# Optimization experiments

Measured on AMD Instinct MI355X. Metric: run time of the kernel, lower is better.

The kernel has to match this reference:

```python
import jax, jax.numpy as jnp
import numpy as np


def _base_grid(B, H, W):
    xs = jnp.arange(W, dtype=jnp.float32)
    ys = jnp.arange(H, dtype=jnp.float32)
    gx, gy = jnp.meshgrid(xs, ys)  # [H,W] each, x varies along W
    return jnp.broadcast_to(jnp.stack([gx, gy], -1)[None], (B, H, W, 2))


def flow_to_grid(flow, accel=None):
    B, _, H, W = flow.shape
    v = 0.5 * flow
    if accel is not None:
        v = v + 0.25 * accel
    vgrid = _base_grid(B, H, W) + jnp.transpose(v, (0, 2, 3, 1))
    gx = 2.0 * vgrid[..., 0] / max(W - 1, 1) - 1.0
    gy = 2.0 * vgrid[..., 1] / max(H - 1, 1) - 1.0
    return jnp.stack([gx, gy], -1)  # [B,H,W,2]


def grid_sample_border(img, grid):
    # img [B,C,H,W], grid [B,Hg,Wg,2] normalized; bilinear, border pad, align_corners=True
    B, C, H, W = img.shape
    Hg, Wg = grid.shape[1], grid.shape[2]
    x = jnp.clip((grid[..., 0] + 1.0) * 0.5 * (W - 1), 0.0, W - 1)
    y = jnp.clip((grid[..., 1] + 1.0) * 0.5 * (H - 1), 0.0, H - 1)
    x0 = jnp.floor(x); y0 = jnp.floor(y)
    x1 = jnp.minimum(x0 + 1.0, W - 1); y1 = jnp.minimum(y0 + 1.0, H - 1)
    wx = (x - x0)[:, None]; wy = (y - y0)[:, None]  # [B,1,Hg,Wg]
    x0i, x1i, y0i, y1i = (a.astype(jnp.int32) for a in (x0, x1, y0, y1))
    flat = img.reshape(B, C, H * W)

    def gat(yi, xi):
        idx = jnp.broadcast_to((yi * W + xi).reshape(B, 1, Hg * Wg), (B, C, Hg * Wg))
        return jnp.take_along_axis(flat, idx, axis=2).reshape(B, C, Hg, Wg)

    v00, v01, v10, v11 = gat(y0i, x0i), gat(y0i, x1i), gat(y1i, x0i), gat(y1i, x1i)
    return v00 * (1 - wx) * (1 - wy) + v01 * wx * (1 - wy) + v10 * (1 - wx) * wy + v11 * wx * wy


def backward_warp(img, flow, accel=None):
    grid = flow_to_grid(flow, accel)
    warped = grid_sample_border(img, grid)
    valid = (jnp.abs(grid[..., 0]) <= 1.0) & (jnp.abs(grid[..., 1]) <= 1.0)
    return warped * valid[:, None].astype(img.dtype)


def local_kernel_warp(img, flow, kernel_params):
    B, C, H, W = img.shape
    k_row = jax.nn.softmax(kernel_params[:, :5], axis=1)   # [B,5,H,W]
    k_col = jax.nn.softmax(kernel_params[:, 5:10], axis=1)
    aniso = jax.nn.sigmoid(kernel_params[:, 10]) + 0.5     # [B,H,W]
    grid = flow_to_grid(flow)                               # [B,H,W,2]
    offsets = jnp.linspace(-2.0, 2.0, 5)
    a3 = aniso[..., None]                                   # [B,H,W,1]
    off_col = offsets.reshape(1, 1, 1, 5) * a3              # [B,H,W,5]
    off_row = offsets.reshape(1, 1, 1, 5) / a3
    zeros = jnp.zeros_like(off_row)
    grid_row = grid[:, :, :, None, :] + jnp.stack([off_row, zeros], -1) * (2.0 / W)
    samples_row = grid_sample_border(img, grid_row.reshape(B, H, W * 5, 2)).reshape(B, C, H, W, 5)
    img_row = jnp.einsum('bchwk,bkhw->bchw', samples_row, k_row)
    grid_base = flow_to_grid(jnp.zeros_like(flow))
    grid_col = grid_base[:, :, :, None, :] + jnp.stack([zeros, off_col], -1) * (2.0 / H)
    samples_col = grid_sample_border(img_row, grid_col.reshape(B, H, W * 5, 2)).reshape(B, C, H, W, 5)
    return jnp.einsum('bchwk,bkhw->bchw', samples_col, k_col)


def conv3x3(x, w, b):
    y = jax.lax.conv_general_dilated(x, w, (1, 1), 'SAME',
                                     dimension_numbers=('NCHW', 'OIHW', 'NCHW'))
    return y + b[None, :, None, None]


def reference(img, features, flow, kernel_params, w1, b1, w2, b2):
    B, _, H, W = img.shape
    Hf, Wf = features.shape[2], features.shape[3]
    warped_img = local_kernel_warp(img, flow, kernel_params)
    flow_scaled = jax.image.resize(flow, (B, 2, Hf, Wf), 'linear') * (Hf / H)
    warped_feat = backward_warp(features, flow_scaled)
    warped_img_down = jax.image.resize(warped_img, (B, 3, Hf, Wf), 'linear')
    x = jnp.concatenate([warped_feat, warped_img_down], axis=1)
    fused = conv3x3(jax.nn.relu(conv3x3(x, w1, b1)), w2, b2)
    return (warped_feat + fused, warped_img)


def setup_inputs() -> dict:
    key = jax.random.key(0)
    ks = jax.random.split(key, 6)
    B, H, W, Hf, Wf, Cf = 4, 512, 512, 256, 256, 96
    return {
        'img': jax.random.uniform(ks[0], (B, 3, H, W), jnp.float32),
        'features': jax.random.normal(ks[1], (B, Cf, Hf, Wf), jnp.float32),
        'flow': jax.random.normal(ks[2], (B, 2, H, W), jnp.float32) * 4.0,
        'kernel_params': jax.random.normal(ks[3], (B, 11, H, W), jnp.float32),
        'w1': jax.random.normal(ks[4], (Cf, Cf + 3, 3, 3), jnp.float32) * 0.02,
        'b1': jnp.zeros((Cf,), jnp.float32),
        'w2': jax.random.normal(ks[5], (Cf, Cf, 3, 3), jnp.float32) * 0.02,
        'b2': jnp.zeros((Cf,), jnp.float32),
    }
```

## Files before the change

### kernel.cpp

```cpp
#include <hip/hip_runtime.h>

#define NB 4
#define IH 512
#define IW 512
#define FH 256
#define FW 256
#define CF 96
#define C1 99
#define HWI (IH*IW)
#define HWF (FH*FW)

typedef short s8v __attribute__((ext_vector_type(8)));
typedef short s4v __attribute__((ext_vector_type(4)));
typedef float f4v __attribute__((ext_vector_type(4)));
typedef float f2v __attribute__((ext_vector_type(2), aligned(4)));

static __device__ __forceinline__ float sigmoidf_(float x) {
    return 1.0f / (1.0f + __expf(-x));
}
static __device__ __forceinline__ unsigned short f2bf(float f) {
    unsigned int u = __float_as_uint(f);
    unsigned int r = (u + 0x7fffu + ((u >> 16) & 1u)) >> 16;
    return (unsigned short)r;
}
static __device__ __forceinline__ float bf2f(short s) {
    unsigned int u = ((unsigned int)(unsigned short)s) << 16;
    return __uint_as_float(u);
}
static __device__ __forceinline__ void gl_lds16(const short* g, short* l) {
    __builtin_amdgcn_global_load_lds(
        (const __attribute__((address_space(1))) void*)g,
        (__attribute__((address_space(3))) void*)l, 16, 0, 0);
}

__global__ __launch_bounds__(256)
void lkw_row_kernel(const float* __restrict__ img,
                    const float* __restrict__ flow,
                    const float* __restrict__ kp,
                    float* __restrict__ img_row) {
    int idx = blockIdx.x * blockDim.x + threadIdx.x;
    if (idx >= NB * HWI) return;
    int w = idx & (IW - 1);
    int h = (idx >> 9) & (IH - 1);
    int b = idx >> 18;

    const float* kpb = kp + (size_t)b * 11 * HWI + h * IW + w;
    float p[5];
    float m = -1e30f;
    #pragma unroll
    for (int k = 0; k < 5; k++) { p[k] = kpb[k * HWI]; m = fmaxf(m, p[k]); }
    float s = 0.f;
    #pragma unroll
    for (int k = 0; k < 5; k++) { p[k] = __expf(p[k] - m); s += p[k]; }
    float invs = 1.f / s;
    float a = sigmoidf_(kpb[10 * HWI]) + 0.5f;
    float inva = 1.f / a;

    float fx = flow[((size_t)b * 2 + 0) * HWI + h * IW + w];
    float fy = flow[((size_t)b * 2 + 1) * HWI + h * IW + w];

    float y = (float)h + 0.5f * fy;
    y = fminf(fmaxf(y, 0.f), (float)(IH - 1));
    float y0f = floorf(y);
    int y0 = (int)y0f;
    int y1 = min(y0 + 1, IH - 1);
    float wy = y - y0f;

    float xbase = (float)w + 0.5f * fx;
    const float sc = (float)(IW - 1) / (float)IW;

    const float* imb = img + (size_t)b * 3 * HWI;
    float acc0 = 0.f, acc1 = 0.f, acc2 = 0.f;
    #pragma unroll
    for (int k = 0; k < 5; k++) {
        float x = xbase + (float)(k - 2) * inva * sc;
        x = fminf(fmaxf(x, 0.f), (float)(IW - 1));
        float x0f = floorf(x);
        int x0 = (int)x0f;
        int x1 = min(x0 + 1, IW - 1);
        float wx = x - x0f;
        float wk = p[k] * invs;
        float w00 = (1.f - wx) * (1.f - wy) * wk;
        float w01 = wx * (1.f - wy) * wk;
        float w10 = (1.f - wx) * wy * wk;
        float w11 = wx * wy * wk;
        int i00 = y0 * IW + x0, i01 = y0 * IW + x1;
        int i10 = y1 * IW + x0, i11 = y1 * IW + x1;
        acc0 += w00 * imb[i00] + w01 * imb[i01] + w10 * imb[i10] + w11 * imb[i11];
        acc1 += w00 * imb[HWI + i00] + w01 * imb[HWI + i01] + w10 * imb[HWI + i10] + w11 * imb[HWI + i11];
        acc2 += w00 * imb[2 * HWI + i00] + w01 * imb[2 * HWI + i01] + w10 * imb[2 * HWI + i10] + w11 * imb[2 * HWI + i11];
    }
    img_row[(size_t)b * 3 * HWI + h * IW + w] = acc0;
    img_row[(size_t)b * 3 * HWI + HWI + h * IW + w] = acc1;
    img_row[(size_t)b * 3 * HWI + 2 * HWI + h * IW + w] = acc2;
}

__global__ __launch_bounds__(256)
void lkw_col_kernel(const float* __restrict__ img_row,
                    const float* __restrict__ kp,
                    float* __restrict__ out1) {
    int idx = blockIdx.x * blockDim.x + threadIdx.x;
    if (idx >= NB * HWI) return;
    int w = idx & (IW - 1);
    int h = (idx >> 9) & (IH - 1);
    int b = idx >> 18;

    const float* kpb = kp + (size_t)b * 11 * HWI + h * IW + w;
    float p[5];
    float m = -1e30f;
    #pragma unroll
    for (int k = 0; k < 5; k++) { p[k] = kpb[(5 + k) * HWI]; m = fmaxf(m, p[k]); }
    float s = 0.f;
    #pragma unroll
    for (int k = 0; k < 5; k++) { p[k] = __expf(p[k] - m); s += p[k]; }
    float invs = 1.f / s;
    float a = sigmoidf_(kpb[10 * HWI]) + 0.5f;

    const float sc = (float)(IH - 1) / (float)IH;
    const float* irb = img_row + (size_t)b * 3 * HWI;
    float acc0 = 0.f, acc1 = 0.f, acc2 = 0.f;
    #pragma unroll
    for (int k = 0; k < 5; k++) {
        float y = (float)h + (float)(k - 2) * a * sc;
        y = fminf(fmaxf(y, 0.f), (float)(IH - 1));
        float y0f = floorf(y);
        int y0 = (int)y0f;
        int y1 = min(y0 + 1, IH - 1);
        float wy = y - y0f;
        float wk = p[k] * invs;
        float w0 = (1.f - wy) * wk, w1 = wy * wk;
        int i0 = y0 * IW + w, i1 = y1 * IW + w;
        acc0 += w0 * irb[i0] + w1 * irb[i1];
        acc1 += w0 * irb[HWI + i0] + w1 * irb[HWI + i1];
        acc2 += w0 * irb[2 * HWI + i0] + w1 * irb[2 * HWI + i1];
    }
    out1[(size_t)b * 3 * HWI + h * IW + w] = acc0;
    out1[(size_t)b * 3 * HWI + HWI + h * IW + w] = acc1;
    out1[(size_t)b * 3 * HWI + 2 * HWI + h * IW + w] = acc2;
}

static __device__ __forceinline__ void ds_taps(int i, int n_in, int t[4], float wt[4]) {
    int n_out = n_in >> 1;
    if (i == 0) {
        t[0] = 0; t[1] = 0; t[2] = 1; t[3] = 2;
        wt[0] = 0.f; wt[1] = 3.f / 7.f; wt[2] = 3.f / 7.f; wt[3] = 1.f / 7.f;
    } else if (i == n_out - 1) {
        t[0] = n_in - 3; t[1] = n_in - 2; t[2] = n_in - 1; t[3] = n_in - 1;
        wt[0] = 1.f / 7.f; wt[1] = 3.f / 7.f; wt[2] = 3.f / 7.f; wt[3] = 0.f;
    } else {
        t[0] = 2 * i - 1; t[1] = 2 * i; t[2] = 2 * i + 1; t[3] = 2 * i + 2;
        wt[0] = 0.125f; wt[1] = 0.375f; wt[2] = 0.375f; wt[3] = 0.125f;
    }
}

__global__ __launch_bounds__(256)
void downsample2x_kernel(const float* __restrict__ src, float* __restrict__ dst,
                         int BC, float mul) {
    int idx = blockIdx.x * blockDim.x + threadIdx.x;
    if (idx >= BC * HWF) return;
    int j = idx & (FW - 1);
    int i = (idx >> 8) & (FH - 1);
    int bc = idx >> 16;

    int tx[4], ty[4];
    float wx[4], wy[4];
    ds_taps(j, IW, tx, wx);
    ds_taps(i, IH, ty, wy);
    const float* s = src + (size_t)bc * HWI;
    float acc = 0.f;
    #pragma unroll
    for (int a = 0; a < 4; a++) {
        if (wy[a] == 0.f) continue;
        const float* rp = s + (size_t)ty[a] * IW;
        float row = wx[0] * rp[tx[0]] + wx[1] * rp[tx[1]] + wx[2] * rp[tx[2]] + wx[3] * rp[tx[3]];
        acc += wy[a] * row;
    }
    dst[idx] = acc * mul;
}

__global__ __launch_bounds__(256)
void imgdown_cl_kernel(const float* __restrict__ out1, short* __restrict__ xin) {
    int idx = blockIdx.x * blockDim.x + threadIdx.x;
    if (idx >= NB * HWF) return;
    int j = idx & (FW - 1);
    int i = (idx >> 8) & (FH - 1);
    int b = idx >> 16;

    int tx[4], ty[4];
    float wx[4], wy[4];
    ds_taps(j, IW, tx, wx);
    ds_taps(i, IH, ty, wy);
    const float* s = out1 + (size_t)b * 3 * HWI;
    float acc[3] = {0.f, 0.f, 0.f};
    #pragma unroll
    for (int a = 0; a < 4; a++) {
        if (wy[a] == 0.f) continue;
        #pragma unroll
        for (int c = 0; c < 3; c++) {
            const float* rp = s + (size_t)c * HWI + (size_t)ty[a] * IW;
            float row = wx[0] * rp[tx[0]] + wx[1] * rp[tx[1]] + wx[2] * rp[tx[2]] + wx[3] * rp[tx[3]];
            acc[c] += wy[a] * row;
        }
    }
    short* dst = xin + ((size_t)(b * FH + i) * FW + j) * 128 + 96;
    s8v g0 = { (short)f2bf(acc[0]), (short)f2bf(acc[1]), (short)f2bf(acc[2]), 0, 0, 0, 0, 0 };
    s8v z  = { 0, 0, 0, 0, 0, 0, 0, 0 };
    *(s8v*)(dst)      = g0;
    *(s8v*)(dst + 8)  = z;
    *(s8v*)(dst + 16) = z;
    *(s8v*)(dst + 24) = z;
}

template <int BF>
__global__ __launch_bounds__(256)
void feat_cl_kernel(const float* __restrict__ feat, void* __restrict__ featT) {
    __shared__ float tile[64 * 97];
    int blk = blockIdx.x;
    int b = blk >> 10;
    int p0 = (blk & 1023) << 6;
    int t = threadIdx.x;
    {
        int px = t & 63, cq = t >> 6;
        const float* src = feat + (size_t)b * CF * HWF + p0 + px;
        #pragma unroll
        for (int k = 0; k < 24; k++) {
            int c = cq * 24 + k;
            tile[px * 97 + c] = src[(size_t)c * HWF];
        }
    }
    __syncthreads();
    int pxo = t >> 2, co = (t & 3) * 24;
    const float* trow = &tile[pxo * 97 + co];
    size_t obase = ((size_t)(b * HWF) + p0 + pxo) * 96 + co;
    if (BF) {
        short* dst = (short*)featT + obase;
        #pragma unroll
        for (int q = 0; q < 3; q++) {
            s8v pk;
            #pragma unroll
            for (int e = 0; e < 8; e++) pk[e] = (short)f2bf(trow[q * 8 + e]);
            *(s8v*)(dst + q * 8) = pk;
        }
    } else {
        float* dst = (float*)featT + obase;
        #pragma unroll
        for (int q = 0; q < 6; q++) {
            f4v vv = { trow[q * 4 + 0], trow[q * 4 + 1], trow[q * 4 + 2], trow[q * 4 + 3] };
            *(f4v*)(dst + q * 4) = vv;
        }
    }
}

template <int BF>
__global__ __launch_bounds__(256)
void warp_feat_cl2_kernel(const void* __restrict__ featT,
                          const float* __restrict__ flow_s,
                          float* __restrict__ wfeat,
                          short* __restrict__ xin) {
    int t = blockIdx.x * 256 + threadIdx.x;
    int g = t & 7;
    int pix = t >> 3;
    int j = pix & (FW - 1);
    int i = (pix >> 8) & (FH - 1);
    int b = pix >> 16;

    float fx = flow_s[((size_t)b * 2 + 0) * HWF + i * FW + j];
    float fy = flow_s[((size_t)b * 2 + 1) * HWF + i * FW + j];
    float u = (float)j + 0.5f * fx;
    float v = (float)i + 0.5f * fy;
    bool valid = (u >= 0.f) && (u <= (float)(FW - 1)) && (v >= 0.f) && (v <= (float)(FH - 1));
    float x = fminf(fmaxf(u, 0.f), (float)(FW - 1));
    float y = fminf(fmaxf(v, 0.f), (float)(FH - 1));
    int x0 = min((int)x, FW - 2);
    int y0 = min((int)y, FH - 2);
    float wxf = x - (float)x0, wyf = y - (float)y0;
    float w00 = (1.f - wxf) * (1.f - wyf), w01 = wxf * (1.f - wyf);
    float w10 = (1.f - wxf) * wyf, w11 = wxf * wyf;
    if (!valid) { w00 = w01 = w10 = w11 = 0.f; }

    size_t base = ((size_t)(b * HWF) + (size_t)y0 * FW + x0) * 96 + g * 12;
    float vals[12];
    if (BF) {
        const short* fp = (const short*)featT + base;
        #pragma unroll
        for (int q = 0; q < 3; q++) {
            s4v a0 = *(const s4v*)(fp + q * 4);
            s4v a1 = *(const s4v*)(fp + 96 + q * 4);
            s4v a2 = *(const s4v*)(fp + 96 * FW + q * 4);
            s4v a3 = *(const s4v*)(fp + 96 * FW + 96 + q * 4);
            #pragma unroll
            for (int e = 0; e < 4; e++)
                vals[q * 4 + e] = w00 * bf2f(a0[e]) + w01 * bf2f(a1[e])
                                + w10 * bf2f(a2[e]) + w11 * bf2f(a3[e]);
        }
    } else {
        const float* fp = (const float*)featT + base;
        #pragma unroll
        for (int q = 0; q < 3; q++) {
            f4v a0 = *(const f4v*)(fp + q * 4);
            f4v a1 = *(const f4v*)(fp + 96 + q * 4);
            f4v a2 = *(const f4v*)(fp + 96 * FW + q * 4);
            f4v a3 = *(const f4v*)(fp + 96 * FW + 96 + q * 4);
            #pragma unroll
            for (int e = 0; e < 4; e++)
                vals[q * 4 + e] = w00 * a0[e] + w01 * a1[e] + w10 * a2[e] + w11 * a3[e];
        }
    }

    float* ob = wfeat + ((size_t)b * CF + g * 12) * HWF + (size_t)i * FW + j;
    #pragma unroll
    for (int k = 0; k < 12; k++) ob[(size_t)k * HWF] = vals[k];

    short* xr = xin + (size_t)pix * 128 + g * 12;
    #pragma unroll
    for (int q2 = 0; q2 < 3; q2++) {
        s4v pk = { (short)f2bf(vals[q2 * 4 + 0]), (short)f2bf(vals[q2 * 4 + 1]),
                   (short)f2bf(vals[q2 * 4 + 2]), (short)f2bf(vals[q2 * 4 + 3]) };
        *(s4v*)(xr + q2 * 4) = pk;
    }
}

__global__ __launch_bounds__(256)
void warp_feat_cl_kernel(const float* __restrict__ feat,
                         const float* __restrict__ flow_s,
                         float* __restrict__ wfeat,
                         short* __restrict__ xin) {
    int t = blockIdx.x * 256 + threadIdx.x;
    int g = t & 7;
    int pix = t >> 3;
    int j = pix & (FW - 1);
    int i = (pix >> 8) & (FH - 1);
    int b = pix >> 16;

    float fx = flow_s[((size_t)b * 2 + 0) * HWF + i * FW + j];
    float fy = flow_s[((size_t)b * 2 + 1) * HWF + i * FW + j];
    float u = (float)j + 0.5f * fx;
    float v = (float)i + 0.5f * fy;
    bool valid = (u >= 0.f) && (u <= (float)(FW - 1)) && (v >= 0.f) && (v <= (float)(FH - 1));
    float x = fminf(fmaxf(u, 0.f), (float)(FW - 1));
    float y = fminf(fmaxf(v, 0.f), (float)(FH - 1));
    int x0 = min((int)x, FW - 2);
    int y0 = min((int)y, FH - 2);
    float wxf = x - (float)x0, wyf = y - (float)y0;
    float w00 = (1.f - wxf) * (1.f - wyf), w01 = wxf * (1.f - wyf);
    float w10 = (1.f - wxf) * wyf, w11 = wxf * wyf;
    if (!valid) { w00 = w01 = w10 = w11 = 0.f; }

    const float* fb = feat + ((size_t)b * CF + g * 12) * HWF + (size_t)y0 * FW + x0;
    float vals[12];
    #pragma unroll
    for (int k = 0; k < 12; k++) {
        const float* p = fb + (size_t)k * HWF;
        f2v r0 = *(const f2v*)p;
        f2v r1 = *(const f2v*)(p + FW);
        vals[k] = w00 * r0.x + w01 * r0.y + w10 * r1.x + w11 * r1.y;
    }

    float* ob = wfeat + ((size_t)b * CF + g * 12) * HWF + (size_t)i * FW + j;
    #pragma unroll
    for (int k = 0; k < 12; k++) ob[(size_t)k * HWF] = vals[k];

    short* xr = xin + (size_t)pix * 128 + g * 12;
    #pragma unroll
    for (int q2 = 0; q2 < 3; q2++) {
        s4v pk = { (short)f2bf(vals[q2 * 4 + 0]), (short)f2bf(vals[q2 * 4 + 1]),
                   (short)f2bf(vals[q2 * 4 + 2]), (short)f2bf(vals[q2 * 4 + 3]) };
        *(s4v*)(xr + q2 * 4) = pk;
    }
}

__global__ __launch_bounds__(256)
void cvt_w1_kernel(const float* __restrict__ w1, short* __restrict__ wA1,
                   short* __restrict__ zpage) {
    int i = blockIdx.x * 256 + threadIdx.x;
    if (i < 128) zpage[i] = 0;
    if (i >= 4 * 3 * 3 * 96 * 32) return;
    int cl = i & 31;
    int co = (i >> 5) % 96;
    int rest = i / 3072;
    int dx = rest % 3;
    int dy = (rest / 3) % 3;
    int kc = rest / 9;
    int ci = kc * 32 + cl;
    float v = (ci < C1) ? w1[((size_t)co * C1 + ci) * 9 + dy * 3 + dx] : 0.f;
    wA1[i] = (short)f2bf(v);
}
__global__ __launch_bounds__(256)
void cvt_w2_kernel(const float* __restrict__ w2, short* __restrict__ wA2) {
    int i = blockIdx.x * 256 + threadIdx.x;
    if (i >= 3 * 3 * 3 * 96 * 32) return;
    int cl = i & 31;
    int co = (i >> 5) % 96;
    int rest = i / 3072;
    int dx = rest % 3;
    int dy = (rest / 3) % 3;
    int kc = rest / 9;
    wA2[i] = (short)f2bf(w2[((size_t)co * CF + kc * 32 + cl) * 9 + dy * 3 + dx]);
}

template <int PASS>
__global__ __launch_bounds__(256)
void conv_mfma5_kernel(const short* __restrict__ X,
                       const short* __restrict__ W,
                       const float* __restrict__ bias,
                       const short* __restrict__ zpage,
                       short* __restrict__ t1out,
                       float* __restrict__ out0) {
    constexpr int KSTR = (PASS == 1) ? 128 : 96;
    constexpr int KC = KSTR / 32;
    constexpr int NSTEP = KC * 3;
    __shared__ short Als[2][320 * 32];
    __shared__ short Bls[2][192 * 32];

    const int bx = blockIdx.x;
    const int w0 = (bx & 1) * 128;
    const int h  = (bx >> 1) & (FH - 1);
    const int b  = bx >> 9;

    const int tid = threadIdx.x;
    const int lane = tid & 63;
    const int wv = tid >> 6;
    const int ln = lane & 15;
    const int q  = lane >> 4;

    f4v acc[6][2];
    #pragma unroll
    for (int mt = 0; mt < 6; mt++)
        #pragma unroll
        for (int nt = 0; nt < 2; nt++)
            acc[mt][nt] = (f4v){0.f, 0.f, 0.f, 0.f};

    const short* Xb = X + (size_t)(b * FH) * FW * KSTR;
    const int bpx = wv * 48 + (lane >> 2);
    const int bch = lane & 3;

    auto issue = [&](int s) {
        const int kcn = s / 3, dyn = s - kcn * 3;
        const int bufn = s & 1;
        const int hy = h + dyn - 1;
        const bool hok = (hy >= 0) && (hy < FH);
        const short* Xrow = Xb + (size_t)(hok ? hy : 0) * FW * KSTR + kcn * 32;
        const short* Wstep = W + (size_t)s * 288 * 32;
        #pragma unroll
        for (int k = 0; k < 5; k++) {
            int c = k * 4 + wv;
            const short* g = (c < 18) ? (Wstep + c * 512 + lane * 8) : zpage;
            gl_lds16(g, &Als[bufn][c * 512]);
        }
        #pragma unroll
        for (int k = 0; k < 3; k++) {
            int px = bpx + k * 16;
            int wp = w0 - 1 + px;
            bool ok = hok && (px < 130) && (wp >= 0) && (wp < FW);
            const short* g = ok ? (Xrow + (size_t)wp * KSTR + bch * 8) : zpage;
            gl_lds16(g, &Bls[bufn][(wv * 48 + k * 16) * 32]);
        }
    };

    issue(0);
    for (int s = 0; s < NSTEP; ++s) {
        if (s + 1 < NSTEP) {
            issue(s + 1);
            asm volatile("s_waitcnt vmcnt(8)" ::: "memory");
        } else {
            asm volatile("s_waitcnt vmcnt(0)" ::: "memory");
        }
        __builtin_amdgcn_s_barrier();
        asm volatile("" ::: "memory");

        const short* Ab = &Als[s & 1][0];
        const short* Bb = &Bls[s & 1][0];
        __builtin_amdgcn_s_setprio(1);
        #pragma unroll
        for (int dx = 0; dx < 3; ++dx) {
            s8v bfr0 = *(const s8v*)(Bb + (wv * 32 + ln + dx) * 32 + q * 8);
            s8v bfr1 = *(const s8v*)(Bb + (wv * 32 + 16 + ln + dx) * 32 + q * 8);
            #pragma unroll
            for (int mt = 0; mt < 6; ++mt) {
                s8v afr = *(const s8v*)(Ab + (dx * 96 + mt * 16 + ln) * 32 + q * 8);
                acc[mt][0] = __builtin_amdgcn_mfma_f32_16x16x32_bf16(afr, bfr0, acc[mt][0], 0, 0, 0);
                acc[mt][1] = __builtin_amdgcn_mfma_f32_16x16x32_bf16(afr, bfr1, acc[mt][1], 0, 0, 0);
            }
        }
        __builtin_amdgcn_s_setprio(0);
        asm volatile("" ::: "memory");
        __builtin_amdgcn_s_barrier();
    }

    if (PASS == 1) {
        const size_t rowbase = (size_t)(b * FH + h) * FW;
        #pragma unroll
        for (int nt = 0; nt < 2; ++nt) {
            int pos = w0 + wv * 32 + nt * 16 + ln;
            short* dst = t1out + (rowbase + pos) * CF;
            #pragma unroll
            for (int mt = 0; mt < 6; ++mt) {
                int co0 = mt * 16 + q * 4;
                s4v pk;
                #pragma unroll
                for (int r = 0; r < 4; ++r) {
                    float v = acc[mt][nt][r] + bias[co0 + r];
                    pk[r] = (short)f2bf(fmaxf(v, 0.f));
                }
                *(s4v*)(dst + co0) = pk;
            }
        }
    } else {
        #pragma unroll
        for (int nt = 0; nt < 2; ++nt) {
            int pos = w0 + wv * 32 + nt * 16 + ln;
            #pragma unroll
            for (int mt = 0; mt < 6; ++mt) {
                int co0 = mt * 16 + q * 4;
                #pragma unroll
                for (int r = 0; r < 4; ++r) {
                    size_t o = (size_t)(b * CF + co0 + r) * HWF + (size_t)h * FW + pos;
                    out0[o] += acc[mt][nt][r] + bias[co0 + r];
                }
            }
        }
    }
}

extern "C" void kernel_launch(void* const* d_in, const int* in_sizes, int n_in,
                              void* d_out, int out_size, void* d_ws, size_t ws_size,
                              hipStream_t stream) {
    const float* img  = (const float*)d_in[0];
    const float* feat = (const float*)d_in[1];
    const float* flow = (const float*)d_in[2];
    const float* kp   = (const float*)d_in[3];
    const float* w1   = (const float*)d_in[4];
    const float* b1   = (const float*)d_in[5];
    const float* w2   = (const float*)d_in[6];
    const float* b2   = (const float*)d_in[7];

    float* out0 = (float*)d_out;
    float* out1 = out0 + (size_t)NB * CF * HWF;

    char* wsb = (char*)d_ws;
    short* wA1 = (short*)wsb;
    short* wA2 = (short*)(wsb + 221184);
    short* zpage = (short*)(wsb + 387072);
    short* xin = (short*)(wsb + 387328);
    const size_t off_after_xin = 387328 + 67108864;

    const size_t FEATT_F32 = (size_t)NB * HWF * 96 * 4;
    const size_t FEATT_BF16 = (size_t)NB * HWF * 96 * 2;
    const size_t FLOW_B = 2097152;
    const size_t need_f32 = off_after_xin + FLOW_B + FEATT_F32;
    const size_t need_b16 = off_after_xin + FLOW_B + FEATT_BF16;

    int n_img = NB * HWI;
    hipLaunchKernelGGL(cvt_w1_kernel, dim3((9 * 96 * 128 + 255) / 256), dim3(256), 0, stream, w1, wA1, zpage);
    hipLaunchKernelGGL(cvt_w2_kernel, dim3((9 * 96 * 96 + 255) / 256), dim3(256), 0, stream, w2, wA2);

    if (ws_size >= need_b16) {
        const bool f32ok = (ws_size >= need_f32);
        float* flow_s = (float*)(wsb + off_after_xin);
        char* region  = wsb + off_after_xin + FLOW_B;
        float* img_row = (float*)region;
        void*  featT   = (void*)region;
        short* t1cl    = (short*)region;

        hipLaunchKernelGGL(lkw_row_kernel, dim3((n_img + 255) / 256), dim3(256), 0, stream,
                           img, flow, kp, img_row);
        hipLaunchKernelGGL(lkw_col_kernel, dim3((n_img + 255) / 256), dim3(256), 0, stream,
                           img_row, kp, out1);
        hipLaunchKernelGGL(downsample2x_kernel, dim3((NB * 2 * HWF + 255) / 256), dim3(256), 0, stream,
                           flow, flow_s, NB * 2, 0.5f);
        hipLaunchKernelGGL(imgdown_cl_kernel, dim3((NB * HWF + 255) / 256), dim3(256), 0, stream,
                           out1, xin);
        if (f32ok) {
            hipLaunchKernelGGL((feat_cl_kernel<0>), dim3(NB * (HWF / 64)), dim3(256), 0, stream,
                               feat, featT);
            hipLaunchKernelGGL((warp_feat_cl2_kernel<0>), dim3(NB * HWF * 8 / 256), dim3(256), 0, stream,
                               featT, flow_s, out0, xin);
        } else {
            hipLaunchKernelGGL((feat_cl_kernel<1>), dim3(NB * (HWF / 64)), dim3(256), 0, stream,
                               feat, featT);
            hipLaunchKernelGGL((warp_feat_cl2_kernel<1>), dim3(NB * HWF * 8 / 256), dim3(256), 0, stream,
                               featT, flow_s, out0, xin);
        }
        hipLaunchKernelGGL((conv_mfma5_kernel<1>), dim3(NB * FH * 2), dim3(256), 0, stream,
                           xin, wA1, b1, zpage, t1cl, (float*)nullptr);
        hipLaunchKernelGGL((conv_mfma5_kernel<2>), dim3(NB * FH * 2), dim3(256), 0, stream,
                           t1cl, wA2, b2, zpage, (short*)nullptr, out0);
    } else {
        char* region = wsb + off_after_xin;
        short* t1cl    = (short*)region;
        float* img_row = (float*)region;
        float* flow_s  = (float*)(region + 16777216);

        hipLaunchKernelGGL(lkw_row_kernel, dim3((n_img + 255) / 256), dim3(256), 0, stream,
                           img, flow, kp, img_row);
        hipLaunchKernelGGL(lkw_col_kernel, dim3((n_img + 255) / 256), dim3(256), 0, stream,
                           img_row, kp, out1);
        hipLaunchKernelGGL(downsample2x_kernel, dim3((NB * 2 * HWF + 255) / 256), dim3(256), 0, stream,
                           flow, flow_s, NB * 2, 0.5f);
        hipLaunchKernelGGL(imgdown_cl_kernel, dim3((NB * HWF + 255) / 256), dim3(256), 0, stream,
                           out1, xin);
        hipLaunchKernelGGL(warp_feat_cl_kernel, dim3(NB * HWF * 8 / 256), dim3(256), 0, stream,
                           feat, flow_s, out0, xin);
        hipLaunchKernelGGL((conv_mfma5_kernel<1>), dim3(NB * FH * 2), dim3(256), 0, stream,
                           xin, wA1, b1, zpage, t1cl, (float*)nullptr);
        hipLaunchKernelGGL((conv_mfma5_kernel<2>), dim3(NB * FH * 2), dim3(256), 0, stream,
                           t1cl, wA2, b2, zpage, (short*)nullptr, out0);
    }
}
```

Measured before the change: 580.5 us.

## Widen conv MFMA tiles to full rows with single-buffered weights and swizzled blocks

The conv kernel now has each block compute a whole 256-pixel row instead of half a row, doubling the N accumulators per wave to 4 tiles. Weights share one LDS buffer while input rows are double-buffered, with the load schedule fully unrolled so the next weights and the input two steps ahead are issued after each compute barrier. Block indices are swizzled, and launch bounds request 3 blocks per CU. The intent is more reuse of each weight fragment, half the halo and weight reloads, and better occupancy, at the cost of more registers, half as many blocks, and less overlap for the weight loads.

```diff
diff --git a/kernel.cpp b/kernel.cpp
--- a/kernel.cpp
+++ b/kernel.cpp
@@ -399,8 +399,8 @@
 }
 
 template <int PASS>
-__global__ __launch_bounds__(256)
-void conv_mfma5_kernel(const short* __restrict__ X,
+__global__ __launch_bounds__(256, 3)
+void conv_mfma6_kernel(const short* __restrict__ X,
                        const short* __restrict__ W,
                        const float* __restrict__ bias,
                        const short* __restrict__ zpage,
@@ -409,13 +409,15 @@
     constexpr int KSTR = (PASS == 1) ? 128 : 96;
     constexpr int KC = KSTR / 32;
     constexpr int NSTEP = KC * 3;
-    __shared__ short Als[2][320 * 32];
-    __shared__ short Bls[2][192 * 32];
-
-    const int bx = blockIdx.x;
-    const int w0 = (bx & 1) * 128;
-    const int h  = (bx >> 1) & (FH - 1);
-    const int b  = bx >> 9;
+    __shared__ short lds[26752];
+    short* const Ab  = lds;
+    short* const Bb0 = lds + 10240;
+    short* const Bb1 = lds + 10240 + 8256;
+
+    const int bx0 = blockIdx.x;
+    const int bx  = (bx0 & 7) * 128 + (bx0 >> 3);
+    const int h   = bx & (FH - 1);
+    const int b   = bx >> 8;
 
     const int tid = threadIdx.x;
     const int lane = tid & 63;
@@ -423,75 +425,110 @@
     const int ln = lane & 15;
     const int q  = lane >> 4;
 
-    f4v acc[6][2];
+    f4v acc[6][4];
     #pragma unroll
     for (int mt = 0; mt < 6; mt++)
         #pragma unroll
-        for (int nt = 0; nt < 2; nt++)
+        for (int nt = 0; nt < 4; nt++)
             acc[mt][nt] = (f4v){0.f, 0.f, 0.f, 0.f};
 
     const short* Xb = X + (size_t)(b * FH) * FW * KSTR;
-    const int bpx = wv * 48 + (lane >> 2);
-    const int bch = lane & 3;
-
-    auto issue = [&](int s) {
-        const int kcn = s / 3, dyn = s - kcn * 3;
-        const int bufn = s & 1;
-        const int hy = h + dyn - 1;
-        const bool hok = (hy >= 0) && (hy < FH);
-        const short* Xrow = Xb + (size_t)(hok ? hy : 0) * FW * KSTR + kcn * 32;
-        const short* Wstep = W + (size_t)s * 288 * 32;
-        #pragma unroll
-        for (int k = 0; k < 5; k++) {
-            int c = k * 4 + wv;
-            const short* g = (c < 18) ? (Wstep + c * 512 + lane * 8) : zpage;
-            gl_lds16(g, &Als[bufn][c * 512]);
-        }
-        #pragma unroll
-        for (int k = 0; k < 3; k++) {
-            int px = bpx + k * 16;
-            int wp = w0 - 1 + px;
-            bool ok = hok && (px < 130) && (wp >= 0) && (wp < FW);
-            const short* g = ok ? (Xrow + (size_t)wp * KSTR + bch * 8) : zpage;
-            gl_lds16(g, &Bls[bufn][(wv * 48 + k * 16) * 32]);
-        }
-    };
-
-    issue(0);
+    const int wp  = wv * 64 + (lane >> 2);
+    const int xof = wp * KSTR + (lane & 3) * 8;
+    bool hokv[3];
+    const short* rowp[3];
+    #pragma unroll
+    for (int dy = 0; dy < 3; dy++) {
+        int hy = h + dy - 1;
+        hokv[dy] = (hy >= 0) && (hy < FH);
+        rowp[dy] = Xb + (size_t)(hokv[dy] ? hy : 0) * FW * KSTR;
+    }
+
+    const int a0 = wv * 5;
+
+    if (tid < 16) {
+        int r = tid >> 2;
+        short* zrow = (r == 0) ? Bb0 : (r == 1) ? (Bb0 + 257 * 32)
+                    : (r == 2) ? Bb1 : (Bb1 + 257 * 32);
+        *(s8v*)(zrow + (tid & 3) * 8) = (s8v){0, 0, 0, 0, 0, 0, 0, 0};
+    }
+    asm volatile("s_waitcnt lgkmcnt(0)" ::: "memory");
+
+    #define ISSUE_B(s_)  {                                                      \
+        constexpr int s = (s_);                                                 \
+        constexpr int kc = s / 3, dy = s % 3;                                   \
+        short* dst = (s & 1) ? Bb1 : Bb0;                                       \
+        const short* rp = rowp[dy];                                             \
+        const bool ok = hokv[dy];                                               \
+        _Pragma("unroll")                                                       \
+        for (int k = 0; k < 4; k++) {                                           \
+            const short* g = ok ? (rp + kc * 32 + xof + k * 16 * KSTR) : zpage; \
+            gl_lds16(g, dst + 32 + (wv * 4 + k) * 512);                         \
+        }                                                                       \
+    }
+    #define ISSUE_A(s_)  {                                                      \
+        constexpr int s = (s_);                                                 \
+        const short* Ws = W + (size_t)s * 9216;                                 \
+        _Pragma("unroll")                                                       \
+        for (int k = 0; k < 5; k++) {                                           \
+            int c = a0 + k;                                                     \
+            const short* g = (c < 18) ? (Ws + c * 512 + lane * 8) : zpage;      \
+            gl_lds16(g, Ab + c * 512);                                          \
+        }                                                                       \
+    }
+
+    ISSUE_B(0);
+    ISSUE_A(0);
+    ISSUE_B(1);
+
+    #pragma unroll
     for (int s = 0; s < NSTEP; ++s) {
-        if (s + 1 < NSTEP) {
-            issue(s + 1);
-            asm volatile("s_waitcnt vmcnt(8)" ::: "memory");
-        } else {
+        if (s < NSTEP - 1)
+            asm volatile("s_waitcnt vmcnt(4)" ::: "memory");
+        else
             asm volatile("s_waitcnt vmcnt(0)" ::: "memory");
-        }
         __builtin_amdgcn_s_barrier();
-        asm volatile("" ::: "memory");
-
-        const short* Ab = &Als[s & 1][0];
-        const short* Bb = &Bls[s & 1][0];
+
+        const short* Bb = (s & 1) ? Bb1 : Bb0;
         __builtin_amdgcn_s_setprio(1);
         #pragma unroll
         for (int dx = 0; dx < 3; ++dx) {
-            s8v bfr0 = *(const s8v*)(Bb + (wv * 32 + ln + dx) * 32 + q * 8);
-            s8v bfr1 = *(const s8v*)(Bb + (wv * 32 + 16 + ln + dx) * 32 + q * 8);
+            s8v bf0 = *(const s8v*)(Bb + (wv * 64 +  0 + ln + dx) * 32 + q * 8);
+            s8v bf1 = *(const s8v*)(Bb + (wv * 64 + 16 + ln + dx) * 32 + q * 8);
+            s8v bf2 = *(const s8v*)(Bb + (wv * 64 + 32 + ln + dx) * 32 + q * 8);
+            s8v bf3 = *(const s8v*)(Bb + (wv * 64 + 48 + ln + dx) * 32 + q * 8);
             #pragma unroll
             for (int mt = 0; mt < 6; ++mt) {
                 s8v afr = *(const s8v*)(Ab + (dx * 96 + mt * 16 + ln) * 32 + q * 8);
-                acc[mt][0] = __builtin_amdgcn_mfma_f32_16x16x32_bf16(afr, bfr0, acc[mt][0], 0, 0, 0);
-                acc[mt][1] = __builtin_amdgcn_mfma_f32_16x16x32_bf16(afr, bfr1, acc[mt][1], 0, 0, 0);
+                acc[mt][0] = __builtin_amdgcn_mfma_f32_16x16x32_bf16(afr, bf0, acc[mt][0], 0, 0, 0);
+                acc[mt][1] = __builtin_amdgcn_mfma_f32_16x16x32_bf16(afr, bf1, acc[mt][1], 0, 0, 0);
+                acc[mt][2] = __builtin_amdgcn_mfma_f32_16x16x32_bf16(afr, bf2, acc[mt][2], 0, 0, 0);
+                acc[mt][3] = __builtin_amdgcn_mfma_f32_16x16x32_bf16(afr, bf3, acc[mt][3], 0, 0, 0);
             }
         }
         __builtin_amdgcn_s_setprio(0);
         asm volatile("" ::: "memory");
         __builtin_amdgcn_s_barrier();
-    }
+
+        switch (s) {
+            #define STAGE_NEXT(ss) case ss: \
+                { if ((ss)+1 < NSTEP) ISSUE_A((ss)+1 < NSTEP ? (ss)+1 : 0); \
+                  if ((ss)+2 < NSTEP) ISSUE_B((ss)+2 < NSTEP ? (ss)+2 : 0); } break;
+            STAGE_NEXT(0) STAGE_NEXT(1) STAGE_NEXT(2) STAGE_NEXT(3)
+            STAGE_NEXT(4) STAGE_NEXT(5) STAGE_NEXT(6) STAGE_NEXT(7)
+            STAGE_NEXT(8) STAGE_NEXT(9) STAGE_NEXT(10) STAGE_NEXT(11)
+            #undef STAGE_NEXT
+            default: break;
+        }
+    }
+    #undef ISSUE_A
+    #undef ISSUE_B
 
     if (PASS == 1) {
         const size_t rowbase = (size_t)(b * FH + h) * FW;
         #pragma unroll
-        for (int nt = 0; nt < 2; ++nt) {
-            int pos = w0 + wv * 32 + nt * 16 + ln;
+        for (int nt = 0; nt < 4; ++nt) {
+            int pos = wv * 64 + nt * 16 + ln;
             short* dst = t1out + (rowbase + pos) * CF;
             #pragma unroll
             for (int mt = 0; mt < 6; ++mt) {
@@ -507,8 +544,8 @@
         }
     } else {
         #pragma unroll
-        for (int nt = 0; nt < 2; ++nt) {
-            int pos = w0 + wv * 32 + nt * 16 + ln;
+        for (int nt = 0; nt < 4; ++nt) {
+            int pos = wv * 64 + nt * 16 + ln;
             #pragma unroll
             for (int mt = 0; mt < 6; ++mt) {
                 int co0 = mt * 16 + q * 4;
@@ -581,9 +618,9 @@
             hipLaunchKernelGGL((warp_feat_cl2_kernel<1>), dim3(NB * HWF * 8 / 256), dim3(256), 0, stream,
                                featT, flow_s, out0, xin);
         }
-        hipLaunchKernelGGL((conv_mfma5_kernel<1>), dim3(NB * FH * 2), dim3(256), 0, stream,
+        hipLaunchKernelGGL((conv_mfma6_kernel<1>), dim3(NB * FH), dim3(256), 0, stream,
                            xin, wA1, b1, zpage, t1cl, (float*)nullptr);
-        hipLaunchKernelGGL((conv_mfma5_kernel<2>), dim3(NB * FH * 2), dim3(256), 0, stream,
+        hipLaunchKernelGGL((conv_mfma6_kernel<2>), dim3(NB * FH), dim3(256), 0, stream,
                            t1cl, wA2, b2, zpage, (short*)nullptr, out0);
     } else {
         char* region = wsb + off_after_xin;
@@ -601,9 +638,9 @@
                            out1, xin);
         hipLaunchKernelGGL(warp_feat_cl_kernel, dim3(NB * HWF * 8 / 256), dim3(256), 0, stream,
                            feat, flow_s, out0, xin);
-        hipLaunchKernelGGL((conv_mfma5_kernel<1>), dim3(NB * FH * 2), dim3(256), 0, stream,
+        hipLaunchKernelGGL((conv_mfma6_kernel<1>), dim3(NB * FH), dim3(256), 0, stream,
                            xin, wA1, b1, zpage, t1cl, (float*)nullptr);
-        hipLaunchKernelGGL((conv_mfma5_kernel<2>), dim3(NB * FH * 2), dim3(256), 0, stream,
+        hipLaunchKernelGGL((conv_mfma6_kernel<2>), dim3(NB * FH), dim3(256), 0, stream,
                            t1cl, wA2, b2, zpage, (short*)nullptr, out0);
     }
 }
```

Result: no change. 583.8 us (+0.6%).
